# Performance work log

Measured on AMD Instinct MI355X. Metric: run time of the kernel, lower is better.

## Reference

```python
import jax, jax.numpy as jnp
import numpy as np

NUM_ITER = 3  # self.num_iter


def setup_inputs() -> dict:
    key = jax.random.key(0)
    k1, k2, k3 = jax.random.split(key, 3)
    B, N, D = 8, 8192, 512          # batch, num_particles, dimension
    P, G, GS = 4, 512, 16           # num projs, groups per proj, group size
    x = jax.random.normal(k1, (B, N, D), dtype=jnp.float32)
    # per-proj feature projection (stand-in for proj.get_delta_x); small scale for stability
    W = jax.random.normal(k2, (P, D, D), dtype=jnp.float32) * 0.02
    groups = jax.random.randint(k3, (P, G, GS), 0, N, dtype=jnp.int32)
    return {"x": x, "W": W, "groups": groups}


def reference(x, W, groups):
    # x: [B, N, D]; W: [P, D, D]; groups: [P, G, GS] indices into N
    B, N, D = x.shape
    P = W.shape[0]
    upd = x
    for ite in range(NUM_ITER):
        scale = 1.0 / (ite + 1)  # ite-dependence of get_delta_x
        delta = jnp.zeros_like(upd)
        for i in range(P):
            g = groups[i]                      # [G, GS]
            gx = upd[:, g, :]                  # gather -> [B, G, GS, D]
            dx = scale * jnp.einsum('bgsd,de->bgse', gx, W[i])
            # scatter-add deltas back onto particle axis (overlaps accumulate)
            delta = delta.at[:, g.reshape(-1), :].add(dx.reshape(B, -1, D))
        upd = upd + delta
    return upd
```

## Files before the change

kernel.cpp:

```cpp
#include <hip/hip_runtime.h>
#include <stdint.h>

#define NROW 8192
#define DDIM 512
#define BB   8
#define PP   4
#define MTOT (BB*NROW)

typedef __attribute__((ext_vector_type(8))) short short8;
typedef __attribute__((ext_vector_type(4))) float floatx4;
typedef __attribute__((ext_vector_type(4))) unsigned int uintx4;

__device__ inline float bf2f(unsigned short h) { return __uint_as_float(((unsigned)h) << 16); }
__device__ inline unsigned short f2bf_rn(float f) {
    return (unsigned short)((__float_as_uint(f) + 0x8000u) >> 16);
}
__device__ inline unsigned pack_bf16(float a, float b) {
    unsigned ua = __float_as_uint(a) + 0x8000u;
    unsigned ub = __float_as_uint(b) + 0x8000u;
    return __builtin_amdgcn_perm(ub, ua, 0x07060302u);
}
__device__ inline uintx4 packA(const floatx4& v0, const floatx4& v1) {
    uintx4 w = { pack_bf16(v0[0], v0[1]), pack_bf16(v0[2], v0[3]),
                 pack_bf16(v1[0], v1[1]), pack_bf16(v1[2], v1[3]) };
    return w;
}

template <typename T> __device__ inline float loadF(const T* p);
template <> __device__ inline float loadF<float>(const float* p) { return *p; }
template <> __device__ inline float loadF<unsigned short>(const unsigned short* p) { return bf2f(*p); }

__device__ inline void glds16(const void* g, void* l) {
    __builtin_amdgcn_global_load_lds(
        (const __attribute__((address_space(1))) void*)g,
        (__attribute__((address_space(3))) void*)l, 16, 0, 0);
}

#define SYNC_VM(N) do {                                                 \
    __builtin_amdgcn_sched_barrier(0);                                  \
    asm volatile("s_waitcnt vmcnt(" #N ") lgkmcnt(0)" ::: "memory");    \
    __builtin_amdgcn_s_barrier();                                       \
    __builtin_amdgcn_sched_barrier(0);                                  \
} while (0)

__global__ void hist_kernel(const int* __restrict__ groups, float* __restrict__ cnt) {
    int t = blockIdx.x * 256 + threadIdx.x;
    int i = t >> 13;
    atomicAdd(&cnt[i * NROW + groups[t]], 1.0f);
}

__global__ void transpose_w(const float* __restrict__ W, unsigned short* __restrict__ Wsw) {
    int u = blockIdx.x * 256 + threadIdx.x;
    int i    = u >> 15;
    int kb   = (u >> 11) & 15;
    int gt   = (u >> 6) & 31;
    int lane = u & 63;
    int n  = gt * 16 + (lane & 15);
    int k0 = kb * 32 + (lane >> 4) * 8;
    const float* wp = W + i * 262144 + k0 * 512 + n;
    unsigned hp[4];
    #pragma unroll
    for (int j = 0; j < 4; ++j)
        hp[j] = pack_bf16(wp[(2*j) * 512], wp[(2*j+1) * 512]);
    uintx4 w = {hp[0], hp[1], hp[2], hp[3]};
    *(uintx4*)(Wsw + (size_t)u * 8) = w;
}

__global__ void cvt_bf16(const float* __restrict__ x, unsigned short* __restrict__ xb) {
    size_t t = (size_t)blockIdx.x * 256 + threadIdx.x;
    const floatx4* p = (const floatx4*)x + t * 2;
    floatx4 v0 = p[0], v1 = p[1];
    *(uintx4*)(xb + t * 8) = packA(v0, v1);
}

template <typename AddT, bool WF32, bool WBF16>
__global__ __launch_bounds__(256, 2)
void gemm_round(const unsigned short* __restrict__ srcA, const AddT* __restrict__ srcAdd,
                const unsigned short* __restrict__ Wsw, const float* __restrict__ cnt,
                float* __restrict__ dstF, unsigned short* __restrict__ dstB, float scale)
{
    __shared__ __align__(16) unsigned char smem[24576];
    float* sE = (float*)smem;

    const int t    = threadIdx.x;
    const int wave = t >> 6;
    const int lane = t & 63;
    const int nb   = blockIdx.x;
    const int m0   = blockIdx.y * 64;

    const int srow = (wave << 4) | (lane & 15);
    const int scol = ((lane >> 4) & 3) * 8;
    const unsigned short* sp = srcA + (size_t)(m0 + srow) * DDIM + scol;

    const unsigned short* bp = Wsw + ((size_t)(wave * 16) * 32 + nb * 4) * 512 + lane * 8;

    floatx4 acc[4][4] = {};
    short8 Bf[4][4];

    auto stage = [&](int buf, int it2) {
        #pragma unroll
        for (int s = 0; s < 2; ++s)
            glds16(sp + (2 * it2 + s) * 32, smem + (buf * 2 + s) * 4096 + wave * 1024);
    };
    auto loadB = [&](int slot, int s) {
        #pragma unroll
        for (int b = 0; b < 4; ++b)
            Bf[slot][b] = *(const short8*)(bp + (size_t)s * 16384 + b * 512);
    };

    stage(0, 0);
    stage(1, 1);
    __builtin_amdgcn_sched_barrier(0);
    loadB(0, 0); loadB(1, 1); loadB(2, 2);
    SYNC_VM(14);

    #pragma unroll
    for (int it = 0; it < 8; ++it) {
        const unsigned short* sAr = (const unsigned short*)(smem + (it % 3) * 8192);

        short8 af[2][4];
        #pragma unroll
        for (int s = 0; s < 2; ++s)
            #pragma unroll
            for (int a = 0; a < 4; ++a)
                af[s][a] = *(const short8*)(sAr + s * 2048 + (a * 64 + lane) * 8);

        if (it < 6) stage((it + 2) % 3, it + 2);
        __builtin_amdgcn_sched_barrier(0);
        if (it < 7) loadB((2 * it + 3) & 3, 2 * it + 3);
        __builtin_amdgcn_sched_barrier(0);

        #pragma unroll
        for (int a = 0; a < 4; ++a)
            #pragma unroll
            for (int b = 0; b < 4; ++b)
                acc[a][b] = __builtin_amdgcn_mfma_f32_16x16x32_bf16(af[0][a], Bf[(2 * it) & 3][b], acc[a][b], 0, 0, 0);

        if (it < 6) loadB((2 * it + 4) & 3, 2 * it + 4);
        __builtin_amdgcn_sched_barrier(0);

        #pragma unroll
        for (int a = 0; a < 4; ++a)
            #pragma unroll
            for (int b = 0; b < 4; ++b)
                acc[a][b] = __builtin_amdgcn_mfma_f32_16x16x32_bf16(af[1][a], Bf[(2 * it + 1) & 3][b], acc[a][b], 0, 0, 0);

        if (it < 6)       SYNC_VM(10);
        else if (it == 6) SYNC_VM(4);
        else              SYNC_VM(0);
    }

    float cs[4][4];
    #pragma unroll
    for (int a = 0; a < 4; ++a)
        #pragma unroll
        for (int q = 0; q < 4; ++q)
            cs[a][q] = cnt[wave * NROW + ((m0 + a * 16 + (lane >> 4) * 4 + q) & (NROW - 1))];

    #pragma unroll
    for (int a = 0; a < 4; ++a) {
        float* se = sE + wave * 1104;
        #pragma unroll
        for (int b = 0; b < 4; ++b)
            #pragma unroll
            for (int q = 0; q < 4; ++q)
                se[((lane >> 4) * 4 + q) * 69 + b * 16 + (lane & 15)] = acc[a][b][q] * cs[a][q];
        __syncthreads();
        #pragma unroll
        for (int e = 0; e < 4; ++e) {
            const int r = wave * 4 + e;
            const size_t m = (size_t)(m0 + a * 16 + r);
            const size_t n = (size_t)nb * 64 + lane;
            const float sum = sE[0 * 1104 + r * 69 + lane] + sE[1 * 1104 + r * 69 + lane]
                            + sE[2 * 1104 + r * 69 + lane] + sE[3 * 1104 + r * 69 + lane];
            const float f = loadF(srcAdd + m * DDIM + n) + scale * sum;
            if constexpr (WF32)  dstF[m * DDIM + n] = f;
            if constexpr (WBF16) dstB[m * DDIM + n] = f2bf_rn(f);
        }
        if (a < 3) __syncthreads();
    }
}

extern "C" void kernel_launch(void* const* d_in, const int* in_sizes, int n_in,
                              void* d_out, int out_size, void* d_ws, size_t ws_size,
                              hipStream_t stream) {
    const float* x      = (const float*)d_in[0];
    const float* W      = (const float*)d_in[1];
    const int*   groups = (const int*)d_in[2];
    float* out = (float*)d_out;

    char* ws = (char*)d_ws;
    float*          cnt = (float*)ws;
    unsigned short* Wsw = (unsigned short*)(ws + 131072);
    unsigned short* U1  = (unsigned short*)(ws + 131072 + 2097152);
    unsigned short* U2  = U1 + (size_t)MTOT * DDIM;

    hipMemsetAsync(cnt, 0, PP * NROW * sizeof(float), stream);
    hist_kernel<<<32768 / 256, 256, 0, stream>>>(groups, cnt);
    transpose_w<<<131072 / 256, 256, 0, stream>>>(W, Wsw);
    cvt_bf16<<<(MTOT * DDIM / 8) / 256, 256, 0, stream>>>(x, U2);

    dim3 grid(DDIM / 64, MTOT / 64);
    gemm_round<float, true, true><<<grid, 256, 0, stream>>>(U2, x, Wsw, cnt, out, U1, 1.0f);
    gemm_round<float, false, true><<<grid, 256, 0, stream>>>(U1, out, Wsw, cnt, nullptr, U2, 0.5f);
    gemm_round<unsigned short, true, false><<<grid, 256, 0, stream>>>(U2, U2, Wsw, cnt, out, nullptr, 1.0f / 3.0f);
}
```

Before: 832.7 us.

## Load A fragments directly to registers, dropping LDS staging and barriers in GEMM loop

Replaces the LDS-staged A operand pipeline (global_load_lds with triple buffering and per-iteration block barriers) with direct per-wave global loads of A fragments into double-buffered registers. MFMA blocks run under raised wave priority, the epilogue's residual add values are prefetched before the reduction, and launch bounds go up to three blocks per CU. Each wave now reads the same A rows redundantly from global or L2 memory instead of sharing them through LDS, and register pressure may limit the higher occupancy target.

Result: slower. 1.153 ms (+38.4%).

```diff
diff --git a/kernel.cpp b/kernel.cpp
--- a/kernel.cpp
+++ b/kernel.cpp
@@ -30,19 +30,6 @@
 template <> __device__ inline float loadF<float>(const float* p) { return *p; }
 template <> __device__ inline float loadF<unsigned short>(const unsigned short* p) { return bf2f(*p); }
 
-__device__ inline void glds16(const void* g, void* l) {
-    __builtin_amdgcn_global_load_lds(
-        (const __attribute__((address_space(1))) void*)g,
-        (__attribute__((address_space(3))) void*)l, 16, 0, 0);
-}
-
-#define SYNC_VM(N) do {                                                 \
-    __builtin_amdgcn_sched_barrier(0);                                  \
-    asm volatile("s_waitcnt vmcnt(" #N ") lgkmcnt(0)" ::: "memory");    \
-    __builtin_amdgcn_s_barrier();                                       \
-    __builtin_amdgcn_sched_barrier(0);                                  \
-} while (0)
-
 __global__ void hist_kernel(const int* __restrict__ groups, float* __restrict__ cnt) {
     int t = blockIdx.x * 256 + threadIdx.x;
     int i = t >> 13;
@@ -74,13 +61,12 @@
 }
 
 template <typename AddT, bool WF32, bool WBF16>
-__global__ __launch_bounds__(256, 2)
+__global__ __launch_bounds__(256, 3)
 void gemm_round(const unsigned short* __restrict__ srcA, const AddT* __restrict__ srcAdd,
                 const unsigned short* __restrict__ Wsw, const float* __restrict__ cnt,
                 float* __restrict__ dstF, unsigned short* __restrict__ dstB, float scale)
 {
-    __shared__ __align__(16) unsigned char smem[24576];
-    float* sE = (float*)smem;
+    __shared__ __align__(16) float sE[4 * 1104];
 
     const int t    = threadIdx.x;
     const int wave = t >> 6;
@@ -88,69 +74,53 @@
     const int nb   = blockIdx.x;
     const int m0   = blockIdx.y * 64;
 
-    const int srow = (wave << 4) | (lane & 15);
-    const int scol = ((lane >> 4) & 3) * 8;
-    const unsigned short* sp = srcA + (size_t)(m0 + srow) * DDIM + scol;
+    const unsigned short* apA[4];
+    #pragma unroll
+    for (int a = 0; a < 4; ++a)
+        apA[a] = srcA + (size_t)(m0 + a * 16 + (lane & 15)) * DDIM + ((lane >> 4) << 3);
 
     const unsigned short* bp = Wsw + ((size_t)(wave * 16) * 32 + nb * 4) * 512 + lane * 8;
 
     floatx4 acc[4][4] = {};
-    short8 Bf[4][4];
-
-    auto stage = [&](int buf, int it2) {
-        #pragma unroll
-        for (int s = 0; s < 2; ++s)
-            glds16(sp + (2 * it2 + s) * 32, smem + (buf * 2 + s) * 4096 + wave * 1024);
-    };
-    auto loadB = [&](int slot, int s) {
-        #pragma unroll
-        for (int b = 0; b < 4; ++b)
-            Bf[slot][b] = *(const short8*)(bp + (size_t)s * 16384 + b * 512);
-    };
-
-    stage(0, 0);
-    stage(1, 1);
-    __builtin_amdgcn_sched_barrier(0);
-    loadB(0, 0); loadB(1, 1); loadB(2, 2);
-    SYNC_VM(14);
+    short8 Ar[2][4], Br[2][4];
 
     #pragma unroll
-    for (int it = 0; it < 8; ++it) {
-        const unsigned short* sAr = (const unsigned short*)(smem + (it % 3) * 8192);
+    for (int a = 0; a < 4; ++a) Ar[0][a] = *(const short8*)(apA[a]);
+    #pragma unroll
+    for (int a = 0; a < 4; ++a) Ar[1][a] = *(const short8*)(apA[a] + 32);
+    #pragma unroll
+    for (int b = 0; b < 4; ++b) Br[0][b] = *(const short8*)(bp + b * 512);
 
-        short8 af[2][4];
-        #pragma unroll
-        for (int s = 0; s < 2; ++s)
+    #pragma unroll
+    for (int kb = 0; kb < 16; ++kb) {
+        if (kb < 15) {
             #pragma unroll
-            for (int a = 0; a < 4; ++a)
-                af[s][a] = *(const short8*)(sAr + s * 2048 + (a * 64 + lane) * 8);
+            for (int b = 0; b < 4; ++b)
+                Br[(kb + 1) & 1][b] = *(const short8*)(bp + (size_t)(kb + 1) * 16384 + b * 512);
+        }
 
-        if (it < 6) stage((it + 2) % 3, it + 2);
-        __builtin_amdgcn_sched_barrier(0);
-        if (it < 7) loadB((2 * it + 3) & 3, 2 * it + 3);
-        __builtin_amdgcn_sched_barrier(0);
-
+        __builtin_amdgcn_s_setprio(1);
         #pragma unroll
         for (int a = 0; a < 4; ++a)
             #pragma unroll
             for (int b = 0; b < 4; ++b)
-                acc[a][b] = __builtin_amdgcn_mfma_f32_16x16x32_bf16(af[0][a], Bf[(2 * it) & 3][b], acc[a][b], 0, 0, 0);
+                acc[a][b] = __builtin_amdgcn_mfma_f32_16x16x32_bf16(Ar[kb & 1][a], Br[kb & 1][b], acc[a][b], 0, 0, 0);
+        __builtin_amdgcn_s_setprio(0);
 
-        if (it < 6) loadB((2 * it + 4) & 3, 2 * it + 4);
-        __builtin_amdgcn_sched_barrier(0);
-
-        #pragma unroll
-        for (int a = 0; a < 4; ++a)
+        if (kb < 14) {
             #pragma unroll
-            for (int b = 0; b < 4; ++b)
-                acc[a][b] = __builtin_amdgcn_mfma_f32_16x16x32_bf16(af[1][a], Bf[(2 * it + 1) & 3][b], acc[a][b], 0, 0, 0);
-
-        if (it < 6)       SYNC_VM(10);
-        else if (it == 6) SYNC_VM(4);
-        else              SYNC_VM(0);
+            for (int a = 0; a < 4; ++a)
+                Ar[kb & 1][a] = *(const short8*)(apA[a] + (kb + 2) * 32);
+        }
     }
 
-    float cs[4][4];
+    float addv[4][4], cs[4][4];
+    #pragma unroll
+    for (int a = 0; a < 4; ++a)
+        #pragma unroll
+        for (int e = 0; e < 4; ++e)
+            addv[a][e] = loadF(srcAdd + (size_t)(m0 + a * 16 + wave * 4 + e) * DDIM
+                                      + (size_t)nb * 64 + lane);
     #pragma unroll
     for (int a = 0; a < 4; ++a)
         #pragma unroll
@@ -173,7 +143,7 @@
             const size_t n = (size_t)nb * 64 + lane;
             const float sum = sE[0 * 1104 + r * 69 + lane] + sE[1 * 1104 + r * 69 + lane]
                             + sE[2 * 1104 + r * 69 + lane] + sE[3 * 1104 + r * 69 + lane];
-            const float f = loadF(srcAdd + m * DDIM + n) + scale * sum;
+            const float f = addv[a][e] + scale * sum;
             if constexpr (WF32)  dstF[m * DDIM + n] = f;
             if constexpr (WBF16) dstB[m * DDIM + n] = f2bf_rn(f);
         }
```
